# Performance work log

Hardware: AMD Instinct MI355X
Metric: run time of the kernel (lower is better)

Reference implementation:

```python
import jax, jax.numpy as jnp
import numpy as np

K = 4                 # max_block_size (depthwise conv kernel size)
BLOCKS = (1, 2, 3, 4) # block sizes, offset 0
DS = 4                # downsample_factor
BLOCK_MULT = 12       # lcm(1,2,3,4)
DIM = 512
NUM_TOKENS = 256


def setup_inputs() -> dict:
    key = jax.random.key(0)
    ks = jax.random.split(key, 8)
    b, n = 4, 4096
    s = 0.02
    return {
        "x": jax.random.randint(ks[0], (b, n), 0, NUM_TOKENS),
        "emb": jax.random.normal(ks[1], (NUM_TOKENS, DIM), dtype=jnp.float32) * s,
        "conv_w": jax.random.normal(ks[2], (DIM, K), dtype=jnp.float32) * s,   # depthwise Conv1d weight [d,1,K] squeezed
        "conv_b": jax.random.normal(ks[3], (DIM,), dtype=jnp.float32) * s,
        "proj_w": jax.random.normal(ks[4], (DIM, DIM), dtype=jnp.float32) * s,  # 1x1 conv == linear [out,in]
        "proj_b": jax.random.normal(ks[5], (DIM,), dtype=jnp.float32) * s,
        "score_w": jax.random.normal(ks[6], (DIM,), dtype=jnp.float32) * s,     # nn.Linear(dim,1)
        "score_b": jax.random.normal(ks[7], (), dtype=jnp.float32) * s,
    }


def reference(x, emb, conv_w, conv_b, proj_w, proj_b, score_w, score_b):
    b, n = x.shape
    h = emb[x]  # [b, n, d] token embedding (gather)

    # pos_conv: pad (K-1) at sequence end, depthwise conv (valid), then pointwise proj
    hp = jnp.pad(h, ((0, 0), (0, K - 1), (0, 0)))
    y = conv_b + sum(hp[:, k:k + n, :] * conv_w[:, k] for k in range(K))  # [b, n, d]
    h = y @ proj_w.T + proj_b

    # pad sequence to multiple of lcm of block sizes
    L = -(-n // BLOCK_MULT) * BLOCK_MULT
    h = jnp.pad(h, ((0, 0), (0, L - n), (0, 0)))

    # multi-scale block mean pooling, upsampled back to length L
    reprs = []
    for bs in BLOCKS:
        r = h.reshape(b, L // bs, bs, DIM).mean(axis=2)     # [b, L/bs, d]
        reprs.append(jnp.repeat(r, bs, axis=1))             # [b, L, d]
    block_reprs = jnp.stack(reprs, axis=2)                  # [b, L, nb, d]

    # per-position block scores
    scores = block_reprs @ score_w + score_b                # [b, L, nb]
    scores = jax.nn.softmax(scores, axis=2)

    # consensus attention over positions (d = nb = len(BLOCKS))
    sim = jnp.einsum('bid,bjd->bij', scores, scores)        # [b, L, L]
    attn = jax.nn.softmax(sim, axis=-1)
    scores = jnp.einsum('bij,bjm->bim', attn, scores)       # [b, L, nb]

    # fuse block representations and downsample
    out = jnp.einsum('bnkd,bnk->bnd', block_reprs, scores)  # [b, L, d]
    m = -(-n // DS) * DS                                    # == n (4096 divisible by 4)
    out = out[:, :m].reshape(b, m // DS, DS, DIM).mean(axis=2)
    return out
```

## Files before the change

### kernel.cpp

```cpp
#include <hip/hip_runtime.h>
#include <hip/hip_bf16.h>

#define B_ 4
#define N_ 4096
#define L_ 4104
#define D_ 512
#define RT 17
#define JC2 32
#define CH2 129
#define BK 64

typedef __attribute__((ext_vector_type(8))) short bf16x8;
typedef __attribute__((ext_vector_type(4))) float f32x4;

#define AS1(p) ((__attribute__((address_space(1))) const void*)(p))
#define AS3(p) ((__attribute__((address_space(3))) void*)(p))

__device__ __forceinline__ float bf2f(unsigned short u) {
  union { unsigned u; float f; } c; c.u = ((unsigned)u) << 16; return c.f;
}

__global__ __launch_bounds__(256) void k_pre(const float* __restrict__ pw,
    __hip_bfloat16* __restrict__ Wbf,
    const int* __restrict__ x, const float* __restrict__ emb,
    const float* __restrict__ conv_w, const float* __restrict__ conv_b,
    unsigned* __restrict__ y) {
  const int bx = blockIdx.x;
  const int t = threadIdx.x;
  if (bx < 1024) {
    const int i = bx * 256 + t;
    Wbf[i] = __float2bfloat16(pw[i]);
    return;
  }
  const int blk = bx - 1024;
  const int b = blk >> 10, i0 = (blk & 1023) * 4;
  const int d = t * 2;
  const float4 c0 = ((const float4*)conv_w)[d];
  const float4 c1 = ((const float4*)conv_w)[d + 1];
  const float ca[4] = {c0.x, c0.y, c0.z, c0.w};
  const float cb[4] = {c1.x, c1.y, c1.z, c1.w};
  const float2 bias2 = ((const float2*)conv_b)[t];

  float2 e[7];
#pragma unroll
  for (int q = 0; q < 7; ++q) e[q] = make_float2(0.f, 0.f);
#pragma unroll
  for (int q = 0; q < 7; ++q) {
    if (i0 + q < N_) {
      const int tok = x[b * N_ + i0 + q];
      e[q] = *(const float2*)(emb + (size_t)tok * D_ + d);
    }
  }
#pragma unroll
  for (int r = 0; r < 4; ++r) {
    float2 acc = bias2;
#pragma unroll
    for (int k = 0; k < 4; ++k) {
      acc.x += e[r + k].x * ca[k];
      acc.y += e[r + k].y * cb[k];
    }
    union { __hip_bfloat16 h[2]; unsigned u; } pk;
    pk.h[0] = __float2bfloat16(acc.x);
    pk.h[1] = __float2bfloat16(acc.y);
    y[(size_t)(b * N_ + i0 + r) * 256 + t] = pk.u;
  }
}

__global__ __launch_bounds__(256) void k_gemm(const __hip_bfloat16* __restrict__ A,
    const __hip_bfloat16* __restrict__ W, const float* __restrict__ bias,
    const float* __restrict__ sw,
    __hip_bfloat16* __restrict__ C, float* __restrict__ tbP) {
  __shared__ __align__(16) __hip_bfloat16 As[2][128 * BK];
  __shared__ __align__(16) __hip_bfloat16 Bs[2][128 * BK];
  const int t = threadIdx.x;
  const int m0 = blockIdx.x * 128, n0 = blockIdx.y * 128;
  const int w = t >> 6, l = t & 63;
  const int quad = l >> 4, r16 = l & 15;
  const int wr = (w >> 1) * 64, wc = (w & 1) * 64;

  f32x4 acc[4][4];
#pragma unroll
  for (int a = 0; a < 4; ++a)
#pragma unroll
    for (int bq = 0; bq < 4; ++bq) acc[a][bq] = (f32x4){0.f, 0.f, 0.f, 0.f};

  const int lr = l >> 3;
  const int lc = ((l & 7) ^ lr) * 8;
  const int arow = m0 + 32 * w + lr;
  const int brow = n0 + 32 * w + lr;
  const int ldsb = 4096 * w;

#define STAGE(buf, kb)                                                            \
  _Pragma("unroll")                                                               \
  for (int ii = 0; ii < 4; ++ii) {                                                \
    __builtin_amdgcn_global_load_lds(                                             \
        AS1(A + (size_t)(arow + 8 * ii) * 512 + (kb) + lc),                       \
        AS3((char*)&As[buf][0] + ldsb + 1024 * ii), 16, 0, 0);                    \
    __builtin_amdgcn_global_load_lds(                                             \
        AS1(W + (size_t)(brow + 8 * ii) * 512 + (kb) + lc),                       \
        AS3((char*)&Bs[buf][0] + ldsb + 1024 * ii), 16, 0, 0);                    \
  }

  STAGE(0, 0)
  __syncthreads();

#pragma unroll 1
  for (int kt = 0; kt < 8; ++kt) {
    const int cur = kt & 1;
    if (kt < 7) { STAGE(1 - cur, (kt + 1) * BK) }
#pragma unroll
    for (int kk = 0; kk < 2; ++kk) {
      const int col_e = (kk * 32 + quad * 8) ^ ((r16 & 7) * 8);
      bf16x8 af[4], bfr[4];
#pragma unroll
      for (int ti = 0; ti < 4; ++ti)
        af[ti] = *(const bf16x8*)(&As[cur][(wr + ti * 16 + r16) * BK + col_e]);
#pragma unroll
      for (int tj = 0; tj < 4; ++tj)
        bfr[tj] = *(const bf16x8*)(&Bs[cur][(wc + tj * 16 + r16) * BK + col_e]);
#pragma unroll
      for (int ti = 0; ti < 4; ++ti)
#pragma unroll
        for (int tj = 0; tj < 4; ++tj)
          acc[ti][tj] = __builtin_amdgcn_mfma_f32_16x16x32_bf16(af[ti], bfr[tj], acc[ti][tj], 0, 0, 0);
    }
    __syncthreads();
  }
#undef STAGE

  float swv[4];
#pragma unroll
  for (int tj = 0; tj < 4; ++tj) swv[tj] = sw[n0 + wc + tj * 16 + r16];

  float tpart[4][4];
#pragma unroll
  for (int ti = 0; ti < 4; ++ti) {
    const int gi0 = m0 + wr + ti * 16 + quad * 4;
#pragma unroll
    for (int r = 0; r < 4; ++r) tpart[ti][r] = 0.f;
#pragma unroll
    for (int tj = 0; tj < 4; ++tj) {
      const int go = n0 + wc + tj * 16 + r16;
      const float bv = bias[go];
#pragma unroll
      for (int r = 0; r < 4; ++r) {
        const float cf = acc[ti][tj][r] + bv;
        C[(size_t)(gi0 + r) * 512 + go] = __float2bfloat16(cf);
        tpart[ti][r] = fmaf(cf, swv[tj], tpart[ti][r]);
      }
    }
  }
#pragma unroll
  for (int ti = 0; ti < 4; ++ti)
#pragma unroll
    for (int r = 0; r < 4; ++r) {
      float v = tpart[ti][r];
      v += __shfl_xor(v, 1); v += __shfl_xor(v, 2);
      v += __shfl_xor(v, 4); v += __shfl_xor(v, 8);
      tpart[ti][r] = v;
    }
  if (r16 == 0) {
    const int p = blockIdx.y * 2 + (w & 1);
#pragma unroll
    for (int ti = 0; ti < 4; ++ti)
#pragma unroll
      for (int r = 0; r < 4; ++r)
        tbP[(size_t)p * 16384 + (m0 + wr + ti * 16 + quad * 4 + r)] = tpart[ti][r];
  }
}

__device__ __forceinline__ float4 softmax4(const float* __restrict__ tw, int base,
                                           int i, float bb) {
  const float s0 = tw[i - base] + bb;
  const int j2 = i & ~1;
  const float s1 = (tw[j2 - base] + tw[j2 + 1 - base]) * 0.5f + bb;
  const int j3 = (i / 3) * 3;
  const float s2 = (tw[j3 - base] + tw[j3 + 1 - base] + tw[j3 + 2 - base]) * (1.f / 3.f) + bb;
  const int j4 = i & ~3;
  const float s3 = (tw[j4 - base] + tw[j4 + 1 - base] + tw[j4 + 2 - base] + tw[j4 + 3 - base]) * 0.25f + bb;
  const float m = fmaxf(fmaxf(s0, s1), fmaxf(s2, s3));
  const float e0 = __expf(s0 - m), e1 = __expf(s1 - m), e2 = __expf(s2 - m), e3 = __expf(s3 - m);
  const float inv = 1.f / (e0 + e1 + e2 + e3);
  return make_float4(e0 * inv, e1 * inv, e2 * inv, e3 * inv);
}

__global__ __launch_bounds__(256) void k_attn(const float* __restrict__ tbP,
    const float* __restrict__ sb,
    float4* __restrict__ accnP, float* __restrict__ accdP) {
  __shared__ float twi[262];
  __shared__ float twj[135];
  __shared__ __align__(16) float4 Sch[CH2];
  const int bx = blockIdx.x;
  const int jc = bx & (JC2 - 1);
  const int rt = (bx >> 5) % RT;
  const int b  = bx / (JC2 * RT);
  const int t = threadIdx.x;
  const int j0 = jc * CH2;
  const int i0 = rt * 256;
  const int rowb = b * N_;
  for (int idx = t; idx < 262; idx += 256) {
    const int j = i0 - 3 + idx;
    float v = 0.f;
    if (j >= 0 && j < N_) {
#pragma unroll
      for (int p = 0; p < 8; ++p) v += tbP[(size_t)p * 16384 + rowb + j];
    }
    twi[idx] = v;
  }
  for (int idx = t; idx < 135; idx += 256) {
    const int j = j0 - 3 + idx;
    float v = 0.f;
    if (j >= 0 && j < N_) {
#pragma unroll
      for (int p = 0; p < 8; ++p) v += tbP[(size_t)p * 16384 + rowb + j];
    }
    twj[idx] = v;
  }
  __syncthreads();
  const float bb = sb[0];
  if (t < CH2 && j0 + t < L_) Sch[t] = softmax4(twj, j0 - 3, j0 + t, bb);
  const int i = i0 + t;
  const float4 si = softmax4(twi, i0 - 3, i, bb);
  __syncthreads();
  if (i < L_) {
    const int len = min(CH2, L_ - j0);
    float l = 0.f, a0 = 0.f, a1 = 0.f, a2 = 0.f, a3 = 0.f;
#pragma unroll 4
    for (int jj = 0; jj < len; ++jj) {
      const float4 v = Sch[jj];
      const float dot = fmaf(si.x, v.x, fmaf(si.y, v.y, fmaf(si.z, v.z, si.w * v.w)));
      const float e = __expf(dot);
      l += e;
      a0 = fmaf(e, v.x, a0); a1 = fmaf(e, v.y, a1);
      a2 = fmaf(e, v.z, a2); a3 = fmaf(e, v.w, a3);
    }
    const size_t base = (size_t)jc * (B_ * L_) + b * L_ + i;
    accnP[base] = make_float4(a0, a1, a2, a3);
    accdP[base] = l;
  }
}

__global__ __launch_bounds__(256) void k_fuse(const __hip_bfloat16* __restrict__ h,
    const float4* __restrict__ accnP, const float* __restrict__ accdP,
    float* __restrict__ out) {
  __shared__ __align__(16) float4 wgtS[12];
  const int bx = blockIdx.x;
  const int b = bx / 342, j12 = bx % 342;
  const int t = threadIdx.x, d = t * 2;
  const int r0 = 12 * j12;

  if (t < 192) {
    const int r = t >> 4, q = t & 15;
    const size_t i1 = (size_t)q * (B_ * L_) + b * L_ + r0 + r;
    const size_t i2 = (size_t)(q + 16) * (B_ * L_) + b * L_ + r0 + r;
    float4 nv = accnP[i1];
    const float4 n2 = accnP[i2];
    nv.x += n2.x; nv.y += n2.y; nv.z += n2.z; nv.w += n2.w;
    float dv = accdP[i1] + accdP[i2];
#pragma unroll
    for (int m = 8; m >= 1; m >>= 1) {
      nv.x += __shfl_xor(nv.x, m); nv.y += __shfl_xor(nv.y, m);
      nv.z += __shfl_xor(nv.z, m); nv.w += __shfl_xor(nv.w, m);
      dv   += __shfl_xor(dv, m);
    }
    if (q == 0) {
      const float inv = 1.f / dv;
      wgtS[r] = make_float4(nv.x * inv, nv.y * inv, nv.z * inv, nv.w * inv);
    }
  }
  __syncthreads();

  const __hip_bfloat16* hb = h + (size_t)b * N_ * D_;
  float2 hv[12];
#pragma unroll
  for (int q = 0; q < 12; ++q) {
    const int row = r0 + q;
    if (row < N_) {
      const ushort2 u = *(const ushort2*)(hb + (size_t)row * D_ + d);
      hv[q] = make_float2(bf2f(u.x), bf2f(u.y));
    } else {
      hv[q] = make_float2(0.f, 0.f);
    }
  }

  float2 p2[6], p3[4], p4[3];
#pragma unroll
  for (int g = 0; g < 6; ++g) {
    p2[g].x = (hv[2 * g].x + hv[2 * g + 1].x) * 0.5f;
    p2[g].y = (hv[2 * g].y + hv[2 * g + 1].y) * 0.5f;
  }
#pragma unroll
  for (int g = 0; g < 4; ++g) {
    p3[g].x = (hv[3 * g].x + hv[3 * g + 1].x + hv[3 * g + 2].x) * (1.f / 3.f);
    p3[g].y = (hv[3 * g].y + hv[3 * g + 1].y + hv[3 * g + 2].y) * (1.f / 3.f);
  }
#pragma unroll
  for (int g = 0; g < 3; ++g) {
    p4[g].x = (hv[4 * g].x + hv[4 * g + 1].x + hv[4 * g + 2].x + hv[4 * g + 3].x) * 0.25f;
    p4[g].y = (hv[4 * g].y + hv[4 * g + 1].y + hv[4 * g + 2].y + hv[4 * g + 3].y) * 0.25f;
  }

#pragma unroll
  for (int o = 0; o < 3; ++o) {
    const int orow = j12 * 3 + o;
    if (orow < 1024) {
      float ox = 0.f, oy = 0.f;
#pragma unroll
      for (int rr = 0; rr < 4; ++rr) {
        const int r = 4 * o + rr;
        const float4 wv = wgtS[r];
        const float2 p1 = hv[r];
        const float2 q2 = p2[r >> 1];
        const float2 q3 = p3[r / 3];
        const float2 q4 = p4[o];
        ox += wv.x * p1.x + wv.y * q2.x + wv.z * q3.x + wv.w * q4.x;
        oy += wv.x * p1.y + wv.y * q2.y + wv.z * q3.y + wv.w * q4.y;
      }
      float2 ov; ov.x = ox * 0.25f; ov.y = oy * 0.25f;
      *(float2*)(out + (size_t)(b * 1024 + orow) * D_ + d) = ov;
    }
  }
}

extern "C" void kernel_launch(void* const* d_in, const int* in_sizes, int n_in,
                              void* d_out, int out_size, void* d_ws, size_t ws_size,
                              hipStream_t stream) {
  const int*   x       = (const int*)d_in[0];
  const float* emb     = (const float*)d_in[1];
  const float* conv_w  = (const float*)d_in[2];
  const float* conv_b  = (const float*)d_in[3];
  const float* proj_w  = (const float*)d_in[4];
  const float* proj_b  = (const float*)d_in[5];
  const float* score_w = (const float*)d_in[6];
  const float* score_b = (const float*)d_in[7];
  float* out = (float*)d_out;

  char* ws = (char*)d_ws;
  size_t off = 0;
  __hip_bfloat16* Wbf = (__hip_bfloat16*)(ws + off); off += (size_t)512 * 512 * 2;
  char*           ybase = ws + off;                  off += (size_t)16384 * 512 * 2;
  __hip_bfloat16* h   = (__hip_bfloat16*)(ws + off); off += (size_t)16384 * 512 * 2;
  float*          tbP = (float*)(ws + off);          off += (size_t)8 * 16384 * 4;
  unsigned* y     = (unsigned*)ybase;
  float4*   accnP = (float4*)ybase;
  float*    accdP = (float*)(ybase + (size_t)JC2 * B_ * L_ * 16);
  (void)in_sizes; (void)n_in; (void)out_size; (void)ws_size;

  k_pre<<<1024 + B_ * N_ / 4, 256, 0, stream>>>(proj_w, Wbf, x, emb, conv_w, conv_b, y);
  k_gemm<<<dim3(128, 4), 256, 0, stream>>>((const __hip_bfloat16*)y, Wbf, proj_b, score_w,
                                           h, tbP);
  k_attn<<<B_ * RT * JC2, 256, 0, stream>>>(tbP, score_b, accnP, accdP);
  k_fuse<<<B_ * 342, 256, 0, stream>>>(h, accnP, accdP, out);
}
```

Baseline: 130.1 us.

## Halve GEMM M-tile to 64 rows and pre-reduce score partials in separate kernel

```diff
diff --git a/kernel.cpp b/kernel.cpp
--- a/kernel.cpp
+++ b/kernel.cpp
@@ -9,6 +9,7 @@
 #define JC2 32
 #define CH2 129
 #define BK 64
+#define NP 16
 
 typedef __attribute__((ext_vector_type(8))) short bf16x8;
 typedef __attribute__((ext_vector_type(4))) float f32x4;
@@ -70,36 +71,36 @@
     const __hip_bfloat16* __restrict__ W, const float* __restrict__ bias,
     const float* __restrict__ sw,
     __hip_bfloat16* __restrict__ C, float* __restrict__ tbP) {
-  __shared__ __align__(16) __hip_bfloat16 As[2][128 * BK];
+  __shared__ __align__(16) __hip_bfloat16 As[2][64 * BK];
   __shared__ __align__(16) __hip_bfloat16 Bs[2][128 * BK];
   const int t = threadIdx.x;
-  const int m0 = blockIdx.x * 128, n0 = blockIdx.y * 128;
+  const int m0 = blockIdx.x * 64, n0 = blockIdx.y * 128;
   const int w = t >> 6, l = t & 63;
   const int quad = l >> 4, r16 = l & 15;
-  const int wr = (w >> 1) * 64, wc = (w & 1) * 64;
-
-  f32x4 acc[4][4];
+  const int wc = w * 32;
+
+  f32x4 acc[4][2];
 #pragma unroll
   for (int a = 0; a < 4; ++a)
 #pragma unroll
-    for (int bq = 0; bq < 4; ++bq) acc[a][bq] = (f32x4){0.f, 0.f, 0.f, 0.f};
+    for (int bq = 0; bq < 2; ++bq) acc[a][bq] = (f32x4){0.f, 0.f, 0.f, 0.f};
 
   const int lr = l >> 3;
   const int lc = ((l & 7) ^ lr) * 8;
-  const int arow = m0 + 32 * w + lr;
-  const int brow = n0 + 32 * w + lr;
-  const int ldsb = 4096 * w;
+  const int rbase = 8 * w + lr;
+  const int ldsb = w * 1024;
 
 #define STAGE(buf, kb)                                                            \
   _Pragma("unroll")                                                               \
-  for (int ii = 0; ii < 4; ++ii) {                                                \
+  for (int ii = 0; ii < 2; ++ii)                                                  \
     __builtin_amdgcn_global_load_lds(                                             \
-        AS1(A + (size_t)(arow + 8 * ii) * 512 + (kb) + lc),                       \
-        AS3((char*)&As[buf][0] + ldsb + 1024 * ii), 16, 0, 0);                    \
+        AS1(A + (size_t)(m0 + 32 * ii + rbase) * 512 + (kb) + lc),                \
+        AS3((char*)&As[buf][0] + ii * 4096 + ldsb), 16, 0, 0);                    \
+  _Pragma("unroll")                                                               \
+  for (int ii = 0; ii < 4; ++ii)                                                  \
     __builtin_amdgcn_global_load_lds(                                             \
-        AS1(W + (size_t)(brow + 8 * ii) * 512 + (kb) + lc),                       \
-        AS3((char*)&Bs[buf][0] + ldsb + 1024 * ii), 16, 0, 0);                    \
-  }
+        AS1(W + (size_t)(n0 + 32 * ii + rbase) * 512 + (kb) + lc),                \
+        AS3((char*)&Bs[buf][0] + ii * 4096 + ldsb), 16, 0, 0);
 
   STAGE(0, 0)
   __syncthreads();
@@ -111,35 +112,35 @@
 #pragma unroll
     for (int kk = 0; kk < 2; ++kk) {
       const int col_e = (kk * 32 + quad * 8) ^ ((r16 & 7) * 8);
-      bf16x8 af[4], bfr[4];
+      bf16x8 af[4], bfr[2];
 #pragma unroll
       for (int ti = 0; ti < 4; ++ti)
-        af[ti] = *(const bf16x8*)(&As[cur][(wr + ti * 16 + r16) * BK + col_e]);
-#pragma unroll
-      for (int tj = 0; tj < 4; ++tj)
+        af[ti] = *(const bf16x8*)(&As[cur][(ti * 16 + r16) * BK + col_e]);
+#pragma unroll
+      for (int tj = 0; tj < 2; ++tj)
         bfr[tj] = *(const bf16x8*)(&Bs[cur][(wc + tj * 16 + r16) * BK + col_e]);
 #pragma unroll
       for (int ti = 0; ti < 4; ++ti)
 #pragma unroll
-        for (int tj = 0; tj < 4; ++tj)
+        for (int tj = 0; tj < 2; ++tj)
           acc[ti][tj] = __builtin_amdgcn_mfma_f32_16x16x32_bf16(af[ti], bfr[tj], acc[ti][tj], 0, 0, 0);
     }
     __syncthreads();
   }
 #undef STAGE
 
-  float swv[4];
-#pragma unroll
-  for (int tj = 0; tj < 4; ++tj) swv[tj] = sw[n0 + wc + tj * 16 + r16];
+  float swv[2];
+#pragma unroll
+  for (int tj = 0; tj < 2; ++tj) swv[tj] = sw[n0 + wc + tj * 16 + r16];
 
   float tpart[4][4];
 #pragma unroll
   for (int ti = 0; ti < 4; ++ti) {
-    const int gi0 = m0 + wr + ti * 16 + quad * 4;
+    const int gi0 = m0 + ti * 16 + quad * 4;
 #pragma unroll
     for (int r = 0; r < 4; ++r) tpart[ti][r] = 0.f;
 #pragma unroll
-    for (int tj = 0; tj < 4; ++tj) {
+    for (int tj = 0; tj < 2; ++tj) {
       const int go = n0 + wc + tj * 16 + r16;
       const float bv = bias[go];
 #pragma unroll
@@ -160,13 +161,22 @@
       tpart[ti][r] = v;
     }
   if (r16 == 0) {
-    const int p = blockIdx.y * 2 + (w & 1);
+    const int p = blockIdx.y * 4 + w;
 #pragma unroll
     for (int ti = 0; ti < 4; ++ti)
 #pragma unroll
       for (int r = 0; r < 4; ++r)
-        tbP[(size_t)p * 16384 + (m0 + wr + ti * 16 + quad * 4 + r)] = tpart[ti][r];
-  }
+        tbP[(size_t)p * 16384 + (m0 + ti * 16 + quad * 4 + r)] = tpart[ti][r];
+  }
+}
+
+__global__ __launch_bounds__(256) void k_tred(const float* __restrict__ tbP,
+                                              float* __restrict__ tb) {
+  const int idx = blockIdx.x * 256 + threadIdx.x;
+  float v = 0.f;
+#pragma unroll
+  for (int p = 0; p < NP; ++p) v += tbP[(size_t)p * 16384 + idx];
+  tb[idx] = v;
 }
 
 __device__ __forceinline__ float4 softmax4(const float* __restrict__ tw, int base,
@@ -184,7 +194,7 @@
   return make_float4(e0 * inv, e1 * inv, e2 * inv, e3 * inv);
 }
 
-__global__ __launch_bounds__(256) void k_attn(const float* __restrict__ tbP,
+__global__ __launch_bounds__(256) void k_attn(const float* __restrict__ tb,
     const float* __restrict__ sb,
     float4* __restrict__ accnP, float* __restrict__ accdP) {
   __shared__ float twi[262];
@@ -200,21 +210,11 @@
   const int rowb = b * N_;
   for (int idx = t; idx < 262; idx += 256) {
     const int j = i0 - 3 + idx;
-    float v = 0.f;
-    if (j >= 0 && j < N_) {
-#pragma unroll
-      for (int p = 0; p < 8; ++p) v += tbP[(size_t)p * 16384 + rowb + j];
-    }
-    twi[idx] = v;
+    twi[idx] = (j >= 0 && j < N_) ? tb[rowb + j] : 0.f;
   }
   for (int idx = t; idx < 135; idx += 256) {
     const int j = j0 - 3 + idx;
-    float v = 0.f;
-    if (j >= 0 && j < N_) {
-#pragma unroll
-      for (int p = 0; p < 8; ++p) v += tbP[(size_t)p * 16384 + rowb + j];
-    }
-    twj[idx] = v;
+    twj[idx] = (j >= 0 && j < N_) ? tb[rowb + j] : 0.f;
   }
   __syncthreads();
   const float bb = sb[0];
@@ -340,15 +340,17 @@
   __hip_bfloat16* Wbf = (__hip_bfloat16*)(ws + off); off += (size_t)512 * 512 * 2;
   char*           ybase = ws + off;                  off += (size_t)16384 * 512 * 2;
   __hip_bfloat16* h   = (__hip_bfloat16*)(ws + off); off += (size_t)16384 * 512 * 2;
-  float*          tbP = (float*)(ws + off);          off += (size_t)8 * 16384 * 4;
+  float*          tbP = (float*)(ws + off);          off += (size_t)NP * 16384 * 4;
+  float*          tb  = (float*)(ws + off);          off += (size_t)16384 * 4;
   unsigned* y     = (unsigned*)ybase;
   float4*   accnP = (float4*)ybase;
   float*    accdP = (float*)(ybase + (size_t)JC2 * B_ * L_ * 16);
   (void)in_sizes; (void)n_in; (void)out_size; (void)ws_size;
 
   k_pre<<<1024 + B_ * N_ / 4, 256, 0, stream>>>(proj_w, Wbf, x, emb, conv_w, conv_b, y);
-  k_gemm<<<dim3(128, 4), 256, 0, stream>>>((const __hip_bfloat16*)y, Wbf, proj_b, score_w,
+  k_gemm<<<dim3(256, 4), 256, 0, stream>>>((const __hip_bfloat16*)y, Wbf, proj_b, score_w,
                                            h, tbP);
-  k_attn<<<B_ * RT * JC2, 256, 0, stream>>>(tbP, score_b, accnP, accdP);
+  k_tred<<<64, 256, 0, stream>>>(tbP, tb);
+  k_attn<<<B_ * RT * JC2, 256, 0, stream>>>(tb, score_b, accnP, accdP);
   k_fuse<<<B_ * 342, 256, 0, stream>>>(h, accnP, accdP, out);
 }
```

After: 135.4 us. +4.1%, slower.

## Precompute per-token projected embeddings per conv tap, replace GEMM with gather-sum

Applied to the files above, without the earlier changes.

```diff
diff --git a/kernel.cpp b/kernel.cpp
--- a/kernel.cpp
+++ b/kernel.cpp
@@ -13,70 +13,36 @@
 typedef __attribute__((ext_vector_type(8))) short bf16x8;
 typedef __attribute__((ext_vector_type(4))) float f32x4;
 
-#define AS1(p) ((__attribute__((address_space(1))) const void*)(p))
-#define AS3(p) ((__attribute__((address_space(3))) void*)(p))
-
 __device__ __forceinline__ float bf2f(unsigned short u) {
   union { unsigned u; float f; } c; c.u = ((unsigned)u) << 16; return c.f;
 }
 
-__global__ __launch_bounds__(256) void k_pre(const float* __restrict__ pw,
-    __hip_bfloat16* __restrict__ Wbf,
-    const int* __restrict__ x, const float* __restrict__ emb,
-    const float* __restrict__ conv_w, const float* __restrict__ conv_b,
-    unsigned* __restrict__ y) {
+__global__ __launch_bounds__(256) void k_g(const float* __restrict__ emb,
+    const float* __restrict__ pw, const float* __restrict__ cwp,
+    const float* __restrict__ cb, const float* __restrict__ pb,
+    float* __restrict__ G, float* __restrict__ biasp) {
   const int bx = blockIdx.x;
   const int t = threadIdx.x;
-  if (bx < 1024) {
-    const int i = bx * 256 + t;
-    Wbf[i] = __float2bfloat16(pw[i]);
+  if (bx >= 32) {
+    const int o = (bx - 32) * 256 + t;
+    const float4* wr = (const float4*)(pw + (size_t)o * 512);
+    const float4* c4 = (const float4*)cb;
+    float s = 0.f;
+    for (int q = 0; q < 128; ++q) {
+      const float4 a = wr[q], c = c4[q];
+      s += a.x * c.x + a.y * c.y + a.z * c.z + a.w * c.w;
+    }
+    biasp[o] = s + pb[o];
     return;
   }
-  const int blk = bx - 1024;
-  const int b = blk >> 10, i0 = (blk & 1023) * 4;
-  const int d = t * 2;
-  const float4 c0 = ((const float4*)conv_w)[d];
-  const float4 c1 = ((const float4*)conv_w)[d + 1];
-  const float ca[4] = {c0.x, c0.y, c0.z, c0.w};
-  const float cb[4] = {c1.x, c1.y, c1.z, c1.w};
-  const float2 bias2 = ((const float2*)conv_b)[t];
-
-  float2 e[7];
-#pragma unroll
-  for (int q = 0; q < 7; ++q) e[q] = make_float2(0.f, 0.f);
-#pragma unroll
-  for (int q = 0; q < 7; ++q) {
-    if (i0 + q < N_) {
-      const int tok = x[b * N_ + i0 + q];
-      e[q] = *(const float2*)(emb + (size_t)tok * D_ + d);
-    }
-  }
-#pragma unroll
-  for (int r = 0; r < 4; ++r) {
-    float2 acc = bias2;
-#pragma unroll
-    for (int k = 0; k < 4; ++k) {
-      acc.x += e[r + k].x * ca[k];
-      acc.y += e[r + k].y * cb[k];
-    }
-    union { __hip_bfloat16 h[2]; unsigned u; } pk;
-    pk.h[0] = __float2bfloat16(acc.x);
-    pk.h[1] = __float2bfloat16(acc.y);
-    y[(size_t)(b * N_ + i0 + r) * 256 + t] = pk.u;
-  }
-}
-
-__global__ __launch_bounds__(256) void k_gemm(const __hip_bfloat16* __restrict__ A,
-    const __hip_bfloat16* __restrict__ W, const float* __restrict__ bias,
-    const float* __restrict__ sw,
-    __hip_bfloat16* __restrict__ C, float* __restrict__ tbP) {
   __shared__ __align__(16) __hip_bfloat16 As[2][128 * BK];
   __shared__ __align__(16) __hip_bfloat16 Bs[2][128 * BK];
-  const int t = threadIdx.x;
-  const int m0 = blockIdx.x * 128, n0 = blockIdx.y * 128;
+  const int m0 = (bx & 1) * 128;
+  const int n0 = ((bx >> 1) & 3) * 128;
+  const int kp = bx >> 3;
   const int w = t >> 6, l = t & 63;
   const int quad = l >> 4, r16 = l & 15;
-  const int wr = (w >> 1) * 64, wc = (w & 1) * 64;
+  const int wr_ = (w >> 1) * 64, wc = (w & 1) * 64;
 
   f32x4 acc[4][4];
 #pragma unroll
@@ -84,37 +50,49 @@
 #pragma unroll
     for (int bq = 0; bq < 4; ++bq) acc[a][bq] = (f32x4){0.f, 0.f, 0.f, 0.f};
 
-  const int lr = l >> 3;
-  const int lc = ((l & 7) ^ lr) * 8;
-  const int arow = m0 + 32 * w + lr;
-  const int brow = n0 + 32 * w + lr;
-  const int ldsb = 4096 * w;
-
-#define STAGE(buf, kb)                                                            \
-  _Pragma("unroll")                                                               \
-  for (int ii = 0; ii < 4; ++ii) {                                                \
-    __builtin_amdgcn_global_load_lds(                                             \
-        AS1(A + (size_t)(arow + 8 * ii) * 512 + (kb) + lc),                       \
-        AS3((char*)&As[buf][0] + ldsb + 1024 * ii), 16, 0, 0);                    \
-    __builtin_amdgcn_global_load_lds(                                             \
-        AS1(W + (size_t)(brow + 8 * ii) * 512 + (kb) + lc),                       \
-        AS3((char*)&Bs[buf][0] + ldsb + 1024 * ii), 16, 0, 0);                    \
-  }
-
-  STAGE(0, 0)
+  const int srow = t >> 1;
+  const int g0 = (t & 1) * 4;
+
+#define STAGEG(buf, kb)                                                        \
+  _Pragma("unroll")                                                            \
+  for (int gi = 0; gi < 4; ++gi) {                                             \
+    const int g = g0 + gi;                                                     \
+    const int c0 = (kb) + g * 8;                                               \
+    const float4 a0 = *(const float4*)(emb + (size_t)(m0 + srow) * 512 + c0);  \
+    const float4 a1 = *(const float4*)(emb + (size_t)(m0 + srow) * 512 + c0 + 4);\
+    const float4 b0 = *(const float4*)(pw + (size_t)(n0 + srow) * 512 + c0);   \
+    const float4 b1 = *(const float4*)(pw + (size_t)(n0 + srow) * 512 + c0 + 4);\
+    union { __hip_bfloat16 q[8]; bf16x8 v; } ua, ub;                           \
+    ua.q[0] = __float2bfloat16(a0.x); ua.q[1] = __float2bfloat16(a0.y);        \
+    ua.q[2] = __float2bfloat16(a0.z); ua.q[3] = __float2bfloat16(a0.w);        \
+    ua.q[4] = __float2bfloat16(a1.x); ua.q[5] = __float2bfloat16(a1.y);        \
+    ua.q[6] = __float2bfloat16(a1.z); ua.q[7] = __float2bfloat16(a1.w);        \
+    float cwv[8];                                                              \
+    _Pragma("unroll")                                                          \
+    for (int e = 0; e < 8; ++e) cwv[e] = cwp[(c0 + e) * 4 + kp];               \
+    ub.q[0] = __float2bfloat16(b0.x * cwv[0]); ub.q[1] = __float2bfloat16(b0.y * cwv[1]);\
+    ub.q[2] = __float2bfloat16(b0.z * cwv[2]); ub.q[3] = __float2bfloat16(b0.w * cwv[3]);\
+    ub.q[4] = __float2bfloat16(b1.x * cwv[4]); ub.q[5] = __float2bfloat16(b1.y * cwv[5]);\
+    ub.q[6] = __float2bfloat16(b1.z * cwv[6]); ub.q[7] = __float2bfloat16(b1.w * cwv[7]);\
+    const int dst = srow * BK + ((g ^ (srow & 7)) * 8);                        \
+    *(bf16x8*)(&As[buf][dst]) = ua.v;                                          \
+    *(bf16x8*)(&Bs[buf][dst]) = ub.v;                                          \
+  }
+
+  STAGEG(0, 0)
   __syncthreads();
 
 #pragma unroll 1
   for (int kt = 0; kt < 8; ++kt) {
     const int cur = kt & 1;
-    if (kt < 7) { STAGE(1 - cur, (kt + 1) * BK) }
+    if (kt < 7) { STAGEG(1 - cur, (kt + 1) * BK) }
 #pragma unroll
     for (int kk = 0; kk < 2; ++kk) {
       const int col_e = (kk * 32 + quad * 8) ^ ((r16 & 7) * 8);
       bf16x8 af[4], bfr[4];
 #pragma unroll
       for (int ti = 0; ti < 4; ++ti)
-        af[ti] = *(const bf16x8*)(&As[cur][(wr + ti * 16 + r16) * BK + col_e]);
+        af[ti] = *(const bf16x8*)(&As[cur][(wr_ + ti * 16 + r16) * BK + col_e]);
 #pragma unroll
       for (int tj = 0; tj < 4; ++tj)
         bfr[tj] = *(const bf16x8*)(&Bs[cur][(wc + tj * 16 + r16) * BK + col_e]);
@@ -126,47 +104,60 @@
     }
     __syncthreads();
   }
-#undef STAGE
-
-  float swv[4];
-#pragma unroll
-  for (int tj = 0; tj < 4; ++tj) swv[tj] = sw[n0 + wc + tj * 16 + r16];
-
-  float tpart[4][4];
+#undef STAGEG
+
 #pragma unroll
   for (int ti = 0; ti < 4; ++ti) {
-    const int gi0 = m0 + wr + ti * 16 + quad * 4;
-#pragma unroll
-    for (int r = 0; r < 4; ++r) tpart[ti][r] = 0.f;
+    const int gi0 = m0 + wr_ + ti * 16 + quad * 4;
 #pragma unroll
     for (int tj = 0; tj < 4; ++tj) {
       const int go = n0 + wc + tj * 16 + r16;
-      const float bv = bias[go];
-#pragma unroll
-      for (int r = 0; r < 4; ++r) {
-        const float cf = acc[ti][tj][r] + bv;
-        C[(size_t)(gi0 + r) * 512 + go] = __float2bfloat16(cf);
-        tpart[ti][r] = fmaf(cf, swv[tj], tpart[ti][r]);
+#pragma unroll
+      for (int r = 0; r < 4; ++r)
+        G[((size_t)kp * 256 + gi0 + r) * 512 + go] = acc[ti][tj][r];
+    }
+  }
+}
+
+__global__ __launch_bounds__(256) void k_h(const int* __restrict__ x,
+    const float* __restrict__ G, const float* __restrict__ biasp,
+    const float* __restrict__ sw, unsigned* __restrict__ h,
+    float* __restrict__ tb) {
+  __shared__ int tokS[11];
+  __shared__ float tpart[8][4];
+  const int bx = blockIdx.x;
+  const int b = bx >> 9, i0 = (bx & 511) * 8;
+  const int t = threadIdx.x, d = t * 2, w = t >> 6, l = t & 63;
+  if (t < 11) {
+    const int j = i0 + t;
+    tokS[t] = (j < N_) ? x[b * N_ + j] : 0;
+  }
+  __syncthreads();
+  const float2 bp  = *(const float2*)(biasp + d);
+  const float2 swv = *(const float2*)(sw + d);
+#pragma unroll
+  for (int r = 0; r < 8; ++r) {
+    const int i = i0 + r;
+    float2 acc = bp;
+#pragma unroll
+    for (int k = 0; k < 4; ++k) {
+      if (i + k < N_) {
+        const float2 g = *(const float2*)(G + ((size_t)k * 256 + tokS[r + k]) * 512 + d);
+        acc.x += g.x; acc.y += g.y;
       }
     }
-  }
-#pragma unroll
-  for (int ti = 0; ti < 4; ++ti)
-#pragma unroll
-    for (int r = 0; r < 4; ++r) {
-      float v = tpart[ti][r];
-      v += __shfl_xor(v, 1); v += __shfl_xor(v, 2);
-      v += __shfl_xor(v, 4); v += __shfl_xor(v, 8);
-      tpart[ti][r] = v;
-    }
-  if (r16 == 0) {
-    const int p = blockIdx.y * 2 + (w & 1);
-#pragma unroll
-    for (int ti = 0; ti < 4; ++ti)
-#pragma unroll
-      for (int r = 0; r < 4; ++r)
-        tbP[(size_t)p * 16384 + (m0 + wr + ti * 16 + quad * 4 + r)] = tpart[ti][r];
-  }
+    union { __hip_bfloat16 q[2]; unsigned u; } pk;
+    pk.q[0] = __float2bfloat16(acc.x);
+    pk.q[1] = __float2bfloat16(acc.y);
+    h[(size_t)(b * N_ + i) * 256 + t] = pk.u;
+    float v = acc.x * swv.x + acc.y * swv.y;
+#pragma unroll
+    for (int off = 32; off > 0; off >>= 1) v += __shfl_xor(v, off);
+    if (l == 0) tpart[r][w] = v;
+  }
+  __syncthreads();
+  if (t < 8)
+    tb[b * N_ + i0 + t] = tpart[t][0] + tpart[t][1] + tpart[t][2] + tpart[t][3];
 }
 
 __device__ __forceinline__ float4 softmax4(const float* __restrict__ tw, int base,
@@ -184,7 +175,7 @@
   return make_float4(e0 * inv, e1 * inv, e2 * inv, e3 * inv);
 }
 
-__global__ __launch_bounds__(256) void k_attn(const float* __restrict__ tbP,
+__global__ __launch_bounds__(256) void k_attn(const float* __restrict__ tb,
     const float* __restrict__ sb,
     float4* __restrict__ accnP, float* __restrict__ accdP) {
   __shared__ float twi[262];
@@ -200,21 +191,11 @@
   const int rowb = b * N_;
   for (int idx = t; idx < 262; idx += 256) {
     const int j = i0 - 3 + idx;
-    float v = 0.f;
-    if (j >= 0 && j < N_) {
-#pragma unroll
-      for (int p = 0; p < 8; ++p) v += tbP[(size_t)p * 16384 + rowb + j];
-    }
-    twi[idx] = v;
+    twi[idx] = (j >= 0 && j < N_) ? tb[rowb + j] : 0.f;
   }
   for (int idx = t; idx < 135; idx += 256) {
     const int j = j0 - 3 + idx;
-    float v = 0.f;
-    if (j >= 0 && j < N_) {
-#pragma unroll
-      for (int p = 0; p < 8; ++p) v += tbP[(size_t)p * 16384 + rowb + j];
-    }
-    twj[idx] = v;
+    twj[idx] = (j >= 0 && j < N_) ? tb[rowb + j] : 0.f;
   }
   __syncthreads();
   const float bb = sb[0];
@@ -337,18 +318,16 @@
 
   char* ws = (char*)d_ws;
   size_t off = 0;
-  __hip_bfloat16* Wbf = (__hip_bfloat16*)(ws + off); off += (size_t)512 * 512 * 2;
-  char*           ybase = ws + off;                  off += (size_t)16384 * 512 * 2;
-  __hip_bfloat16* h   = (__hip_bfloat16*)(ws + off); off += (size_t)16384 * 512 * 2;
-  float*          tbP = (float*)(ws + off);          off += (size_t)8 * 16384 * 4;
-  unsigned* y     = (unsigned*)ybase;
-  float4*   accnP = (float4*)ybase;
-  float*    accdP = (float*)(ybase + (size_t)JC2 * B_ * L_ * 16);
+  float*          G    = (float*)(ws + off);          off += (size_t)4 * 256 * 512 * 4;
+  float*          bias = (float*)(ws + off);          off += (size_t)512 * 4;
+  __hip_bfloat16* h    = (__hip_bfloat16*)(ws + off); off += (size_t)16384 * 512 * 2;
+  float*          tb   = (float*)(ws + off);          off += (size_t)16384 * 4;
+  float4*         accnP = (float4*)(ws + off);        off += (size_t)JC2 * B_ * L_ * 16;
+  float*          accdP = (float*)(ws + off);         off += (size_t)JC2 * B_ * L_ * 4;
   (void)in_sizes; (void)n_in; (void)out_size; (void)ws_size;
 
-  k_pre<<<1024 + B_ * N_ / 4, 256, 0, stream>>>(proj_w, Wbf, x, emb, conv_w, conv_b, y);
-  k_gemm<<<dim3(128, 4), 256, 0, stream>>>((const __hip_bfloat16*)y, Wbf, proj_b, score_w,
-                                           h, tbP);
-  k_attn<<<B_ * RT * JC2, 256, 0, stream>>>(tbP, score_b, accnP, accdP);
+  k_g<<<34, 256, 0, stream>>>(emb, proj_w, conv_w, conv_b, proj_b, G, bias);
+  k_h<<<2048, 256, 0, stream>>>(x, G, bias, score_w, (unsigned*)h, tb);
+  k_attn<<<B_ * RT * JC2, 256, 0, stream>>>(tb, score_b, accnP, accdP);
   k_fuse<<<B_ * 342, 256, 0, stream>>>(h, accnP, accdP, out);
 }
```

Result: slower. 149.2 us (+14.7%).
